# Optimization experiments

Hardware: AMD Instinct MI355X
Metric: run time of the kernel (lower is better)

## Reference

```python
import jax, jax.numpy as jnp
import numpy as np

# ---- config (YOLOv4-style, TRAIN_SIZE=608, P2..P5) ----
STRIDES = (4.0, 8.0, 16.0, 32.0)
ANCHORS = np.array([
    [[12, 16], [19, 36], [40, 28], [36, 75]],
    [[36, 75], [76, 55], [72, 146], [142, 110]],
    [[72, 146], [142, 110], [192, 243], [459, 401]],
    [[142, 110], [192, 243], [300, 300], [459, 401]],
], dtype=np.float32)  # [LEVELS, NUM_ANCHORS, 2]
MAX_PROP = 100
SCORE_THRESH = 0.25
IOU_THRESH = 0.5


def decode_prediction(p, anchors, stride):
    # p: [b, A, h, w, 6] -> [b, A*h*w, 5] with xyxy + score
    b, A, h, w, _ = p.shape
    txy, twh, conf, cls = p[..., :2], p[..., 2:4], p[..., 4:5], p[..., 5:6]
    gx, gy = jnp.meshgrid(jnp.arange(w, dtype=p.dtype), jnp.arange(h, dtype=p.dtype))
    grid = jnp.stack([gx, gy], axis=-1)[None, None]  # [1,1,h,w,2]
    xy = (jax.nn.sigmoid(txy) + grid) * stride
    wh = jnp.exp(twh) * anchors[None, :, None, None, :]
    score = jax.nn.sigmoid(conf) * jax.nn.sigmoid(cls)
    x1y1 = xy - 0.5 * wh
    x2y2 = xy + 0.5 * wh
    out = jnp.concatenate([x1y1, x2y2, score], axis=-1)  # [b,A,h,w,5]
    return out.reshape(b, A * h * w, 5)


def _iou_one_vs_all(box, boxes):
    # box: [4], boxes: [N,4] (xyxy)
    lt = jnp.maximum(box[:2], boxes[:, :2])
    rb = jnp.minimum(box[2:], boxes[:, 2:])
    wh = jnp.maximum(rb - lt, 0.0)
    inter = wh[:, 0] * wh[:, 1]
    a1 = jnp.maximum(box[2] - box[0], 0.0) * jnp.maximum(box[3] - box[1], 0.0)
    a2 = jnp.maximum(boxes[:, 2] - boxes[:, 0], 0.0) * jnp.maximum(boxes[:, 3] - boxes[:, 1], 0.0)
    return inter / (a1 + a2 - inter + 1e-9)


def _nms_single(boxes, scores):
    # greedy NMS, padded to MAX_PROP with zero rows
    s0 = jnp.where(scores >= SCORE_THRESH, scores, 0.0)

    def step(s, _):
        i = jnp.argmax(s)
        sc = s[i]
        box = boxes[i]
        keep = sc > 0.0
        row = jnp.where(keep, jnp.concatenate([box, sc[None]]), jnp.zeros(5, boxes.dtype))
        iou = _iou_one_vs_all(box, boxes)
        s = jnp.where((iou > IOU_THRESH) & keep, 0.0, s)
        s = s.at[i].set(0.0)
        return s, row

    _, props = jax.lax.scan(step, s0, None, length=MAX_PROP)
    return props  # [MAX_PROP, 5]


def entry_stop_gradients(t, mask):
    # gradient flows only through entries where mask==1
    return jax.lax.stop_gradient(t) * (1.0 - mask) + t * mask


def _forward(p2, p3, p4, p5):
    anchors = jnp.asarray(ANCHORS)
    d2 = decode_prediction(p2, anchors[0], STRIDES[0])
    d3 = decode_prediction(p3, anchors[1], STRIDES[1])
    d4 = decode_prediction(p4, anchors[2], STRIDES[2])
    d5 = decode_prediction(p5, anchors[3], STRIDES[3])
    proposals = jnp.concatenate([d2, d3, d4, d5], axis=1)  # [b, N, 5]
    proposals = jax.vmap(lambda pr: _nms_single(pr[:, :4], pr[:, 4]))(proposals)  # [b, MAX_PROP, 5]
    mask = (jnp.sum(proposals[..., :4], axis=-1) != 0.0).astype(proposals.dtype)[..., None]
    return entry_stop_gradients(proposals, mask)


def setup_inputs() -> dict:
    key = jax.random.key(0)
    k2, k3, k4, k5 = jax.random.split(key, 4)
    b, A, ch = 32, 4, 6
    return {
        "p2": jax.random.normal(k2, (b, A, 152, 152, ch), dtype=jnp.float32),
        "p3": jax.random.normal(k3, (b, A, 76, 76, ch), dtype=jnp.float32),
        "p4": jax.random.normal(k4, (b, A, 38, 38, ch), dtype=jnp.float32),
        "p5": jax.random.normal(k5, (b, A, 19, 19, ch), dtype=jnp.float32),
    }


def reference(p2, p3, p4, p5):
    return _forward(p2, p3, p4, p5)
```

## Files before the change

kernel.cpp:

```cpp
#include <hip/hip_runtime.h>
#include <cstdint>
#include <cstddef>

typedef unsigned int u32;
typedef unsigned long long u64;

#define NTOT 122740
#define NQ   (NTOT / 4)
#define KTOP 1024
#define WIN  256
#define SCORE_T 0.25f
#define TBITS 0x3E800000u


__device__ __forceinline__ float sigm(float x) { return 1.0f / (1.0f + expf(-x)); }

__device__ float4 decode_box_from_gidx(u32 gidx, int b,
    const float* __restrict__ p2, const float* __restrict__ p3,
    const float* __restrict__ p4, const float* __restrict__ p5)
{
  const float* p; int t, H, W; float stride;
  float aw0, ah0, aw1, ah1, aw2, ah2, aw3, ah3;
  if (gidx < 92416u) {
    p = p2 + (size_t)b * 92416 * 6; t = (int)gidx; H = 152; W = 152; stride = 4.0f;
    aw0=12.f; ah0=16.f; aw1=19.f; ah1=36.f; aw2=40.f; ah2=28.f; aw3=36.f; ah3=75.f;
  } else if (gidx < 115520u) {
    p = p3 + (size_t)b * 23104 * 6; t = (int)(gidx - 92416u); H = 76; W = 76; stride = 8.0f;
    aw0=36.f; ah0=75.f; aw1=76.f; ah1=55.f; aw2=72.f; ah2=146.f; aw3=142.f; ah3=110.f;
  } else if (gidx < 121296u) {
    p = p4 + (size_t)b * 5776 * 6; t = (int)(gidx - 115520u); H = 38; W = 38; stride = 16.0f;
    aw0=72.f; ah0=146.f; aw1=142.f; ah1=110.f; aw2=192.f; ah2=243.f; aw3=459.f; ah3=401.f;
  } else {
    p = p5 + (size_t)b * 1444 * 6; t = (int)(gidx - 121296u); H = 19; W = 19; stride = 32.0f;
    aw0=142.f; ah0=110.f; aw1=192.f; ah1=243.f; aw2=300.f; ah2=300.f; aw3=459.f; ah3=401.f;
  }
  int HW = H * W;
  int a = t / HW;
  int r = t - a * HW;
  int y = r / W;
  int x = r - y * W;
  const float* q = p + (size_t)t * 6;
  float2 t01 = *(const float2*)(q + 0);
  float2 t23 = *(const float2*)(q + 2);
  float cx = (sigm(t01.x) + (float)x) * stride;
  float cy = (sigm(t01.y) + (float)y) * stride;
  float aw = (a == 0) ? aw0 : (a == 1) ? aw1 : (a == 2) ? aw2 : aw3;
  float ah = (a == 0) ? ah0 : (a == 1) ? ah1 : (a == 2) ? ah2 : ah3;
  float bw = expf(t23.x) * aw;
  float bh = expf(t23.y) * ah;
  return make_float4(cx - 0.5f * bw, cy - 0.5f * bh, cx + 0.5f * bw, cy + 0.5f * bh);
}

__device__ __forceinline__ bool iou_gt(float4 A, float4 B) {
  float ltx = fmaxf(A.x, B.x), lty = fmaxf(A.y, B.y);
  float rbx = fminf(A.z, B.z), rby = fminf(A.w, B.w);
  float w = fmaxf(rbx - ltx, 0.0f), h = fmaxf(rby - lty, 0.0f);
  float inter = w * h;
  float a1 = fmaxf(A.z - A.x, 0.0f) * fmaxf(A.w - A.y, 0.0f);
  float a2 = fmaxf(B.z - B.x, 0.0f) * fmaxf(B.w - B.y, 0.0f);
  float iou = inter / (a1 + a2 - inter + 1e-9f);
  return iou > 0.5f;
}

__device__ __forceinline__ int score_bin(u32 bits) {
  return min(4095, 1 + (int)((bits - TBITS) >> 12));
}

__global__ __launch_bounds__(256)
void decode_scores_kernel(const float* __restrict__ p2, const float* __restrict__ p3,
                          const float* __restrict__ p4, const float* __restrict__ p5,
                          u32* __restrict__ scores)
{
  int t = blockIdx.x * 256 + threadIdx.x;
  int b = blockIdx.y;
  if (t >= NTOT) return;
  const float* q;
  if (t < 92416)       q = p2 + ((size_t)b * 92416 + (size_t)t) * 6;
  else if (t < 115520) q = p3 + ((size_t)b * 23104 + (size_t)(t - 92416)) * 6;
  else if (t < 121296) q = p4 + ((size_t)b * 5776  + (size_t)(t - 115520)) * 6;
  else                 q = p5 + ((size_t)b * 1444  + (size_t)(t - 121296)) * 6;
  float2 cc = *(const float2*)(q + 4);
  float s = sigm(cc.x) * sigm(cc.y);
  scores[(size_t)b * NTOT + t] = (s >= SCORE_T) ? __float_as_uint(s) : 0u;
}

__global__ __launch_bounds__(1024, 1)
void topk_nms_kernel(const u32* __restrict__ scores,
                     const float* __restrict__ p2, const float* __restrict__ p3,
                     const float* __restrict__ p4, const float* __restrict__ p5,
                     float* __restrict__ out)
{
  const int b = blockIdx.x;
  const int tid = threadIdx.x;
  const uint4* sp = (const uint4*)(scores + (size_t)b * NTOT);

  __shared__ u64 skey[KTOP];
  __shared__ u32 hist[4096];
  __shared__ u32 scanbuf[1024];
  __shared__ float4 sbox[WIN];
  __shared__ u64 smat[WIN * 4];
  __shared__ float4 selbox[100];
  __shared__ int s_misc[4];

  for (int i = tid; i < 4096; i += 1024) hist[i] = 0u;
  if (tid == 0) { s_misc[1] = 0; s_misc[3] = 0; }
  __syncthreads();
  for (int i = tid; i < NQ; i += 1024) {
    uint4 v = sp[i];
    if (v.x >= TBITS) atomicAdd(&hist[score_bin(v.x)], 1u);
    if (v.y >= TBITS) atomicAdd(&hist[score_bin(v.y)], 1u);
    if (v.z >= TBITS) atomicAdd(&hist[score_bin(v.z)], 1u);
    if (v.w >= TBITS) atomicAdd(&hist[score_bin(v.w)], 1u);
  }
  __syncthreads();

  u32 g = hist[4 * tid] + hist[4 * tid + 1] + hist[4 * tid + 2] + hist[4 * tid + 3];
  scanbuf[tid] = g;
  __syncthreads();
  for (int off = 1; off < 1024; off <<= 1) {
    u32 v = (tid + off < 1024) ? scanbuf[tid + off] : 0u;
    __syncthreads();
    scanbuf[tid] += v;
    __syncthreads();
  }

  if (tid == 0 && scanbuf[0] <= (u32)KTOP) s_misc[0] = 0;
  {
    u32 nxt = (tid < 1023) ? scanbuf[tid + 1] : 0u;
    if (scanbuf[tid] > (u32)KTOP && nxt <= (u32)KTOP) {
      u32 c = nxt;
      int B = 4 * tid + 4;
      for (int bin = 4 * tid + 3; bin >= 4 * tid; --bin) {
        c += hist[bin];
        if (c <= (u32)KTOP) B = bin; else break;
      }
      s_misc[0] = B;
    }
  }
  __syncthreads();
  const int B = max(s_misc[0], 1);

  for (int i = tid; i < NQ; i += 1024) {
    uint4 v = sp[i];
    u32 c4[4] = { v.x, v.y, v.z, v.w };
    #pragma unroll
    for (int c = 0; c < 4; ++c) {
      u32 bits = c4[c];
      if (bits >= TBITS && score_bin(bits) >= B) {
        int pos = atomicAdd(&s_misc[1], 1);
        if (pos < KTOP) {
          u32 gidx = (u32)(4 * i + c);
          skey[pos] = ~(((u64)bits << 32) | (u32)(~gidx));
        }
      }
    }
  }
  __syncthreads();
  const int n = min(s_misc[1], KTOP);
  for (int i = tid; i < KTOP; i += 1024)
    if (i >= n) skey[i] = ~0ull;
  __syncthreads();

  for (int kk = 2; kk <= KTOP; kk <<= 1) {
    for (int jj = kk >> 1; jj > 0; jj >>= 1) {
      int i = tid;
      int ixj = i ^ jj;
      if (ixj > i) {
        u64 a = skey[i], c = skey[ixj];
        bool up = ((i & kk) == 0);
        if ((a > c) == up) { skey[i] = c; skey[ixj] = a; }
      }
      __syncthreads();
    }
  }

  const int W = min(n, WIN);

  if (tid < WIN) {
    if (tid < W) {
      u32 gidx = ~(u32)(~skey[tid]);
      sbox[tid] = decode_box_from_gidx(gidx, b, p2, p3, p4, p5);
    } else {
      sbox[tid] = make_float4(0.f, 0.f, 0.f, 0.f);
    }
  }
  __syncthreads();

  {
    int row = tid >> 2, word = tid & 3;
    u64 bits = 0;
    if (row < W) {
      float4 A = sbox[row];
      int j0 = word * 64;
      int jend = min(64, W - j0);
      for (int j = 0; j < jend; ++j)
        if (iou_gt(A, sbox[j0 + j])) bits |= (1ull << j);
    }
    smat[tid] = bits;
  }
  __syncthreads();

  if (tid == 0) {
    u64 s0 = 0, s1 = 0, s2 = 0, s3 = 0;
    int sel = 0;
    for (int p = 0; p < W && sel < 100; ++p) {
      u64 sw = (p < 64) ? s0 : (p < 128) ? s1 : (p < 192) ? s2 : s3;
      if ((sw >> (p & 63)) & 1ull) continue;
      float4 box = sbox[p];
      u64 kcomp = ~skey[p];
      float sc = __uint_as_float((u32)(kcomp >> 32));
      selbox[sel] = box;
      float* orow = out + (size_t)b * 500 + (size_t)sel * 5;
      orow[0] = box.x; orow[1] = box.y; orow[2] = box.z; orow[3] = box.w; orow[4] = sc;
      sel++;
      s0 |= smat[p * 4 + 0]; s1 |= smat[p * 4 + 1];
      s2 |= smat[p * 4 + 2]; s3 |= smat[p * 4 + 3];
    }
    s_misc[2] = sel;
    s_misc[3] = (sel < 100 && n > WIN) ? 1 : 0;
  }
  __syncthreads();

  if (s_misc[3]) {
    if (tid < 64) {
      const int lane = tid;
      int sel = s_misc[2];
      for (int p = WIN; p < n && sel < 100; ++p) {
        u64 kcomp = ~skey[p];
        u32 gidx = ~(u32)kcomp;
        float4 box = decode_box_from_gidx(gidx, b, p2, p3, p4, p5);
        bool hit = false;
        if (lane < sel) hit = iou_gt(selbox[lane], box);
        if (lane + 64 < sel) hit = hit || iou_gt(selbox[lane + 64], box);
        u64 anyhit = __ballot(hit);
        if (anyhit == 0ull) {
          if (lane == 0) {
            selbox[sel] = box;
            float sc = __uint_as_float((u32)(kcomp >> 32));
            float* orow = out + (size_t)b * 500 + (size_t)sel * 5;
            orow[0] = box.x; orow[1] = box.y; orow[2] = box.z; orow[3] = box.w; orow[4] = sc;
          }
          sel++;
        }
      }
      if (lane == 0) s_misc[2] = sel;
    }
  }
  __syncthreads();

  const int nsel = s_misc[2];
  for (int i = tid; i < (100 - nsel) * 5; i += 1024)
    out[(size_t)b * 500 + (size_t)nsel * 5 + i] = 0.0f;
}

extern "C" void kernel_launch(void* const* d_in, const int* in_sizes, int n_in,
                              void* d_out, int out_size, void* d_ws, size_t ws_size,
                              hipStream_t stream) {
  const float* p2 = (const float*)d_in[0];
  const float* p3 = (const float*)d_in[1];
  const float* p4 = (const float*)d_in[2];
  const float* p5 = (const float*)d_in[3];
  float* out = (float*)d_out;

  u32* scores = (u32*)d_ws;

  decode_scores_kernel<<<dim3(480, 32), 256, 0, stream>>>(p2, p3, p4, p5, scores);
  topk_nms_kernel<<<32, 1024, 0, stream>>>(scores, p2, p3, p4, p5, out);
}
```

Measured before the change: 192.4 us.

## Split histogram and threshold filtering across many blocks per batch

```diff
diff --git a/kernel.cpp b/kernel.cpp
--- a/kernel.cpp
+++ b/kernel.cpp
@@ -6,14 +6,25 @@
 typedef unsigned long long u64;
 
 #define NTOT 122740
-#define NQ   (NTOT / 4)
+#define NQ   30685
+#define NPAIR 61370
 #define KTOP 1024
 #define WIN  256
+#define NBIN 4096
 #define SCORE_T 0.25f
 #define TBITS 0x3E800000u
-
+#define CSTRIDE 64
+
+
+#define WS_COUNTERS 524288
+#define WS_COMPACT  532480
+#define WS_SCORES   794624
 
 __device__ __forceinline__ float sigm(float x) { return 1.0f / (1.0f + expf(-x)); }
+
+__device__ __forceinline__ int score_bin(u32 bits) {
+  return min(4095, 1 + (int)((bits - TBITS) >> 12));
+}
 
 __device__ float4 decode_box_from_gidx(u32 gidx, int b,
     const float* __restrict__ p2, const float* __restrict__ p3,
@@ -62,109 +73,155 @@
   return iou > 0.5f;
 }
 
-__device__ __forceinline__ int score_bin(u32 bits) {
-  return min(4095, 1 + (int)((bits - TBITS) >> 12));
+__global__ __launch_bounds__(1024)
+void zero_kernel(u32* w) {
+  int t = blockIdx.x * 1024 + threadIdx.x;
+  if (t < 133120) w[t] = 0u;
 }
 
 __global__ __launch_bounds__(256)
-void decode_scores_kernel(const float* __restrict__ p2, const float* __restrict__ p3,
-                          const float* __restrict__ p4, const float* __restrict__ p5,
-                          u32* __restrict__ scores)
+void decode_score_hist(const float* __restrict__ p2, const float* __restrict__ p3,
+                       const float* __restrict__ p4, const float* __restrict__ p5,
+                       u32* __restrict__ scores, u32* __restrict__ hist)
 {
-  int t = blockIdx.x * 256 + threadIdx.x;
-  int b = blockIdx.y;
-  if (t >= NTOT) return;
-  const float* q;
-  if (t < 92416)       q = p2 + ((size_t)b * 92416 + (size_t)t) * 6;
-  else if (t < 115520) q = p3 + ((size_t)b * 23104 + (size_t)(t - 92416)) * 6;
-  else if (t < 121296) q = p4 + ((size_t)b * 5776  + (size_t)(t - 115520)) * 6;
-  else                 q = p5 + ((size_t)b * 1444  + (size_t)(t - 121296)) * 6;
-  float2 cc = *(const float2*)(q + 4);
-  float s = sigm(cc.x) * sigm(cc.y);
-  scores[(size_t)b * NTOT + t] = (s >= SCORE_T) ? __float_as_uint(s) : 0u;
+  __shared__ u32 lhist[NBIN];
+  const int tid = threadIdx.x;
+  const int b = blockIdx.y;
+  for (int i = tid; i < NBIN; i += 256) lhist[i] = 0u;
+  __syncthreads();
+
+  uint2* srow = (uint2*)(scores + (size_t)b * NTOT);
+  const int pbase = blockIdx.x * 2048;
+  #pragma unroll 2
+  for (int k = 0; k < 8; ++k) {
+    int P = pbase + k * 256 + tid;
+    if (P < NPAIR) {
+      int t0 = 2 * P;
+      const float* p; int l0, LN;
+      if (t0 < 92416)       { p = p2; l0 = t0;          LN = 92416; }
+      else if (t0 < 115520) { p = p3; l0 = t0 - 92416;  LN = 23104; }
+      else if (t0 < 121296) { p = p4; l0 = t0 - 115520; LN = 5776;  }
+      else                  { p = p5; l0 = t0 - 121296; LN = 1444;  }
+      const float* q = p + ((size_t)b * LN + (size_t)l0) * 6 + 4;
+      float4 v1 = *(const float4*)(q);
+      float4 v2 = *(const float4*)(q + 4);
+      float s0 = sigm(v1.x) * sigm(v1.y);
+      float s1 = sigm(v2.z) * sigm(v2.w);
+      u32 b0 = (s0 >= SCORE_T) ? __float_as_uint(s0) : 0u;
+      u32 b1 = (s1 >= SCORE_T) ? __float_as_uint(s1) : 0u;
+      srow[P] = make_uint2(b0, b1);
+      if (b0) atomicAdd(&lhist[score_bin(b0)], 1u);
+      if (b1) atomicAdd(&lhist[score_bin(b1)], 1u);
+    }
+  }
+  __syncthreads();
+  u32* gh = hist + (size_t)b * NBIN;
+  for (int i = tid; i < NBIN; i += 256) {
+    u32 v = lhist[i];
+    if (v) atomicAdd(&gh[i], v);
+  }
+}
+
+__global__ __launch_bounds__(256)
+void filter_kernel(const u32* __restrict__ scores, const u32* __restrict__ hist,
+                   u32* __restrict__ counters, uint2* __restrict__ compact)
+{
+  __shared__ u32 shist[NBIN];
+  __shared__ u32 scan[256];
+  __shared__ uint2 cand[KTOP];
+  __shared__ u32 s_cnt, s_base;
+  __shared__ int s_B;
+  const int tid = threadIdx.x;
+  const int b = blockIdx.y;
+
+  const u32* gh = hist + (size_t)b * NBIN;
+  for (int i = tid; i < NBIN; i += 256) shist[i] = gh[i];
+  if (tid == 0) s_cnt = 0u;
+  __syncthreads();
+
+  u32 g = 0;
+  const int base = tid * 16;
+  #pragma unroll
+  for (int k = 0; k < 16; ++k) g += shist[base + k];
+  scan[tid] = g;
+  __syncthreads();
+  for (int off = 1; off < 256; off <<= 1) {
+    u32 v = (tid + off < 256) ? scan[tid + off] : 0u;
+    __syncthreads();
+    scan[tid] += v;
+    __syncthreads();
+  }
+  if (tid == 0 && scan[0] <= (u32)KTOP) s_B = 1;
+  {
+    u32 nxt = (tid < 255) ? scan[tid + 1] : 0u;
+    if (scan[tid] > (u32)KTOP && nxt <= (u32)KTOP) {
+      u32 c = nxt;
+      int Bv = base + 16;
+      for (int bin = base + 15; bin >= base; --bin) {
+        c += shist[bin];
+        if (c <= (u32)KTOP) Bv = bin; else break;
+      }
+      s_B = Bv;
+    }
+  }
+  __syncthreads();
+  const int B = max(s_B, 1);
+
+  const uint4* sp = (const uint4*)(scores + (size_t)b * NTOT);
+  const int i0 = blockIdx.x * 2048;
+  const int i1 = min(i0 + 2048, NQ);
+  for (int i = i0 + tid; i < i1; i += 256) {
+    uint4 v = sp[i];
+    u32 c4[4] = { v.x, v.y, v.z, v.w };
+    #pragma unroll
+    for (int c = 0; c < 4; ++c) {
+      u32 bits = c4[c];
+      if (bits && score_bin(bits) >= B) {
+        u32 pos = atomicAdd(&s_cnt, 1u);
+        if (pos < (u32)KTOP) cand[pos] = make_uint2(bits, (u32)(4 * i + c));
+      }
+    }
+  }
+  __syncthreads();
+  const u32 m = min(s_cnt, (u32)KTOP);
+  if (tid == 0) s_base = m ? atomicAdd(&counters[(size_t)b * CSTRIDE], m) : 0u;
+  __syncthreads();
+  const u32 gbase = s_base;
+  uint2* crow = compact + (size_t)b * KTOP;
+  for (u32 i = tid; i < m; i += 256) {
+    u32 dst = gbase + i;
+    if (dst < (u32)KTOP) crow[dst] = cand[i];
+  }
 }
 
 __global__ __launch_bounds__(1024, 1)
-void topk_nms_kernel(const u32* __restrict__ scores,
+void sort_nms_kernel(const uint2* __restrict__ compact, const u32* __restrict__ counters,
                      const float* __restrict__ p2, const float* __restrict__ p3,
                      const float* __restrict__ p4, const float* __restrict__ p5,
                      float* __restrict__ out)
 {
   const int b = blockIdx.x;
   const int tid = threadIdx.x;
-  const uint4* sp = (const uint4*)(scores + (size_t)b * NTOT);
 
   __shared__ u64 skey[KTOP];
-  __shared__ u32 hist[4096];
-  __shared__ u32 scanbuf[1024];
   __shared__ float4 sbox[WIN];
   __shared__ u64 smat[WIN * 4];
   __shared__ float4 selbox[100];
   __shared__ int s_misc[4];
 
-  for (int i = tid; i < 4096; i += 1024) hist[i] = 0u;
-  if (tid == 0) { s_misc[1] = 0; s_misc[3] = 0; }
-  __syncthreads();
-  for (int i = tid; i < NQ; i += 1024) {
-    uint4 v = sp[i];
-    if (v.x >= TBITS) atomicAdd(&hist[score_bin(v.x)], 1u);
-    if (v.y >= TBITS) atomicAdd(&hist[score_bin(v.y)], 1u);
-    if (v.z >= TBITS) atomicAdd(&hist[score_bin(v.z)], 1u);
-    if (v.w >= TBITS) atomicAdd(&hist[score_bin(v.w)], 1u);
-  }
-  __syncthreads();
-
-  u32 g = hist[4 * tid] + hist[4 * tid + 1] + hist[4 * tid + 2] + hist[4 * tid + 3];
-  scanbuf[tid] = g;
-  __syncthreads();
-  for (int off = 1; off < 1024; off <<= 1) {
-    u32 v = (tid + off < 1024) ? scanbuf[tid + off] : 0u;
-    __syncthreads();
-    scanbuf[tid] += v;
-    __syncthreads();
-  }
-
-  if (tid == 0 && scanbuf[0] <= (u32)KTOP) s_misc[0] = 0;
-  {
-    u32 nxt = (tid < 1023) ? scanbuf[tid + 1] : 0u;
-    if (scanbuf[tid] > (u32)KTOP && nxt <= (u32)KTOP) {
-      u32 c = nxt;
-      int B = 4 * tid + 4;
-      for (int bin = 4 * tid + 3; bin >= 4 * tid; --bin) {
-        c += hist[bin];
-        if (c <= (u32)KTOP) B = bin; else break;
-      }
-      s_misc[0] = B;
-    }
-  }
-  __syncthreads();
-  const int B = max(s_misc[0], 1);
-
-  for (int i = tid; i < NQ; i += 1024) {
-    uint4 v = sp[i];
-    u32 c4[4] = { v.x, v.y, v.z, v.w };
-    #pragma unroll
-    for (int c = 0; c < 4; ++c) {
-      u32 bits = c4[c];
-      if (bits >= TBITS && score_bin(bits) >= B) {
-        int pos = atomicAdd(&s_misc[1], 1);
-        if (pos < KTOP) {
-          u32 gidx = (u32)(4 * i + c);
-          skey[pos] = ~(((u64)bits << 32) | (u32)(~gidx));
-        }
-      }
-    }
-  }
-  __syncthreads();
-  const int n = min(s_misc[1], KTOP);
-  for (int i = tid; i < KTOP; i += 1024)
-    if (i >= n) skey[i] = ~0ull;
+  const int n = min((int)counters[(size_t)b * CSTRIDE], KTOP);
+  const uint2* crow = compact + (size_t)b * KTOP;
+  if (tid < n) {
+    uint2 pr = crow[tid];
+    skey[tid] = ~(((u64)pr.x << 32) | (u32)(~pr.y));
+  } else {
+    skey[tid] = ~0ull;
+  }
   __syncthreads();
 
   for (int kk = 2; kk <= KTOP; kk <<= 1) {
     for (int jj = kk >> 1; jj > 0; jj >>= 1) {
-      int i = tid;
-      int ixj = i ^ jj;
+      int i = tid, ixj = i ^ jj;
       if (ixj > i) {
         u64 a = skey[i], c = skey[ixj];
         bool up = ((i & kk) == 0);
@@ -174,26 +231,22 @@
     }
   }
 
-  const int W = min(n, WIN);
+  const int Wn = min(n, WIN);
 
   if (tid < WIN) {
-    if (tid < W) {
-      u32 gidx = ~(u32)(~skey[tid]);
-      sbox[tid] = decode_box_from_gidx(gidx, b, p2, p3, p4, p5);
-    } else {
-      sbox[tid] = make_float4(0.f, 0.f, 0.f, 0.f);
-    }
+    sbox[tid] = (tid < Wn) ? decode_box_from_gidx(~(u32)(~skey[tid]), b, p2, p3, p4, p5)
+                           : make_float4(0.f, 0.f, 0.f, 0.f);
   }
   __syncthreads();
 
   {
     int row = tid >> 2, word = tid & 3;
     u64 bits = 0;
-    if (row < W) {
+    if (row < Wn) {
       float4 A = sbox[row];
       int j0 = word * 64;
-      int jend = min(64, W - j0);
-      for (int j = 0; j < jend; ++j)
+      int je = min(64, Wn - j0);
+      for (int j = 0; j < je; ++j)
         if (iou_gt(A, sbox[j0 + j])) bits |= (1ull << j);
     }
     smat[tid] = bits;
@@ -203,7 +256,7 @@
   if (tid == 0) {
     u64 s0 = 0, s1 = 0, s2 = 0, s3 = 0;
     int sel = 0;
-    for (int p = 0; p < W && sel < 100; ++p) {
+    for (int p = 0; p < Wn && sel < 100; ++p) {
       u64 sw = (p < 64) ? s0 : (p < 128) ? s1 : (p < 192) ? s2 : s3;
       if ((sw >> (p & 63)) & 1ull) continue;
       float4 box = sbox[p];
@@ -227,8 +280,7 @@
       int sel = s_misc[2];
       for (int p = WIN; p < n && sel < 100; ++p) {
         u64 kcomp = ~skey[p];
-        u32 gidx = ~(u32)kcomp;
-        float4 box = decode_box_from_gidx(gidx, b, p2, p3, p4, p5);
+        float4 box = decode_box_from_gidx(~(u32)kcomp, b, p2, p3, p4, p5);
         bool hit = false;
         if (lane < sel) hit = iou_gt(selbox[lane], box);
         if (lane + 64 < sel) hit = hit || iou_gt(selbox[lane + 64], box);
@@ -262,8 +314,14 @@
   const float* p5 = (const float*)d_in[3];
   float* out = (float*)d_out;
 
-  u32* scores = (u32*)d_ws;
-
-  decode_scores_kernel<<<dim3(480, 32), 256, 0, stream>>>(p2, p3, p4, p5, scores);
-  topk_nms_kernel<<<32, 1024, 0, stream>>>(scores, p2, p3, p4, p5, out);
-}
+  unsigned char* w = (unsigned char*)d_ws;
+  u32*   hist     = (u32*)w;
+  u32*   counters = (u32*)(w + WS_COUNTERS);
+  uint2* compact  = (uint2*)(w + WS_COMPACT);
+  u32*   scores   = (u32*)(w + WS_SCORES);
+
+  zero_kernel<<<130, 1024, 0, stream>>>(hist);
+  decode_score_hist<<<dim3(30, 32), 256, 0, stream>>>(p2, p3, p4, p5, scores, hist);
+  filter_kernel<<<dim3(15, 32), 256, 0, stream>>>(scores, hist, counters, compact);
+  sort_nms_kernel<<<32, 1024, 0, stream>>>(compact, counters, p2, p3, p4, p5, out);
+}
```

Result: faster. 180.6 us (-6.1%).
